# Performance work log

Hardware: AMD Instinct MI355X
Metric: run time of the kernel (lower is better)

## Reference

```python
import jax, jax.numpy as jnp
import numpy as np

N_NODES = 50000
N_EDGES = 1600000
HID = 128
REST = 96  # (hidden//4) x 1e vectors = 32*3
N_MP = 2


def _linear_init(key, fan_in, fan_out):
    return jax.random.normal(key, (fan_in, fan_out), dtype=jnp.float32) / np.sqrt(fan_in)


def setup_inputs() -> dict:
    key = jax.random.key(0)
    ks = jax.random.split(key, 16)
    h = jax.random.normal(ks[0], (N_NODES, HID + REST), dtype=jnp.float32)
    edge_index = jax.random.randint(ks[1], (2, N_EDGES), 0, N_NODES, dtype=jnp.int32)
    edge_len = jax.random.uniform(ks[2], (N_EDGES,), dtype=jnp.float32) * 5.0
    # ScalarMessagePassing MLPs: Linear(2*HID+1 -> HID), SiLU, Linear(HID -> HID), stacked per layer
    mp_w1 = jnp.stack([_linear_init(ks[3 + i], 2 * HID + 1, HID) for i in range(N_MP)])
    mp_b1 = jnp.zeros((N_MP, HID), dtype=jnp.float32)
    mp_w2 = jnp.stack([_linear_init(ks[5 + i], HID, HID) for i in range(N_MP)])
    mp_b2 = jnp.zeros((N_MP, HID), dtype=jnp.float32)
    # NodeUpdateMLP: Linear(HID -> HID), SiLU, Linear(HID -> HID)
    nu_w1 = _linear_init(ks[7], HID, HID)
    nu_b1 = jnp.zeros((HID,), dtype=jnp.float32)
    nu_w2 = _linear_init(ks[8], HID, HID)
    nu_b2 = jnp.zeros((HID,), dtype=jnp.float32)
    return dict(h=h, edge_index=edge_index, edge_len=edge_len,
                mp_w1=mp_w1, mp_b1=mp_b1, mp_w2=mp_w2, mp_b2=mp_b2,
                nu_w1=nu_w1, nu_b1=nu_b1, nu_w2=nu_w2, nu_b2=nu_b2)


def _scalar_mp(scalars, sender, receiver, edge_len, w1, b1, w2, b2):
    # gather -> MLP -> index_add scatter, residual on scalar channels
    msg_in = jnp.concatenate([scalars[sender], scalars[receiver], edge_len[:, None]], axis=-1)  # [E, 2H+1]
    msgs = jax.nn.silu(msg_in @ w1 + b1) @ w2 + b2  # [E, H]
    agg = jax.ops.segment_sum(msgs, receiver, num_segments=scalars.shape[0])  # [N, H]
    return scalars + agg


def reference(h, edge_index, edge_len, mp_w1, mp_b1, mp_w2, mp_b2, nu_w1, nu_b1, nu_w2, nu_b2):
    scalars, rest = h[..., :HID], h[..., HID:]
    sender, receiver = edge_index[0], edge_index[1]
    for i in range(N_MP):
        scalars = _scalar_mp(scalars, sender, receiver, edge_len,
                             mp_w1[i], mp_b1[i], mp_w2[i], mp_b2[i])
    # NodeUpdateMLP: scalars + MLP(scalars)
    scalars = scalars + (jax.nn.silu(scalars @ nu_w1 + nu_b1) @ nu_w2 + nu_b2)
    return jnp.concatenate([scalars, rest], axis=-1)
```

## Files before the change

### kernel.cpp

```cpp
#include <hip/hip_runtime.h>
#include <hip/hip_fp16.h>


#define NFEAT 224
#define RBITS 8
#define NB 196
#define CAP 10240
#define COPYB 512

typedef _Float16 v8h __attribute__((ext_vector_type(8)));
typedef _Float16 v2h __attribute__((ext_vector_type(2)));
typedef float f32x4 __attribute__((ext_vector_type(4)));

#define MFMA16(a, b, c) __builtin_amdgcn_mfma_f32_16x16x32_f16(a, b, c, 0, 0, 0)

__device__ __forceinline__ float silu_f(float x) {
    float e = __expf(-x);
    return x * __builtin_amdgcn_rcpf(1.0f + e);
}

__global__ void k_packbucket(const float* __restrict__ mp_w1, const float* __restrict__ mp_w2,
                             const float* __restrict__ nu_w1, const float* __restrict__ nu_w2,
                             _Float16* __restrict__ Wp,
                             const int* __restrict__ recv, const int* __restrict__ sender,
                             const float* __restrict__ elen, int* __restrict__ cnt,
                             uint2* __restrict__ bp, int E) {
    __shared__ int lhist[256];
    __shared__ int lcur[256];
    if (blockIdx.x < 8) {
        const float* srcs[8] = {
            mp_w1, mp_w1 + 16384, mp_w2,
            mp_w1 + 32896, mp_w1 + 32896 + 16384, mp_w2 + 16384,
            nu_w1, nu_w2
        };
        const float* W = srcs[blockIdx.x];
        _Float16* dst = Wp + (size_t)blockIdx.x * 16384;
        for (int i = 0; i < 8; ++i) {
            int u = threadIdx.x + i * 256;
            int nt = u >> 8;
            int kt = (u >> 6) & 3;
            int lane = u & 63;
            int kb = kt * 32 + (lane >> 4) * 8;
            int n = nt * 16 + (lane & 15);
#pragma unroll
            for (int j = 0; j < 8; ++j)
                dst[(size_t)u * 8 + j] = (_Float16)W[(size_t)(kb + j) * 128 + n];
        }
        return;
    }
    int t = threadIdx.x;
    int start = (blockIdx.x - 8) * 4096;
    int end = start + 4096; if (end > E) end = E;
    lhist[t] = 0;
    __syncthreads();
    int rv[16];
#pragma unroll
    for (int j = 0; j < 16; ++j) {
        int i = start + t + j * 256;
        rv[j] = (i < end) ? recv[i] : -1;
        if (rv[j] >= 0) atomicAdd(&lhist[rv[j] >> RBITS], 1);
    }
    __syncthreads();
    if (t < NB) {
        int c = lhist[t];
        lcur[t] = t * CAP + (c ? atomicAdd(&cnt[t], c) : 0);
    }
    __syncthreads();
#pragma unroll
    for (int j = 0; j < 16; ++j) {
        int i = start + t + j * 256;
        if (i < end) {
            int r = rv[j];
            int pos = atomicAdd(&lcur[r >> RBITS], 1);
            unsigned pay = (unsigned)sender[i] |
                           ((unsigned)__half_as_ushort(__float2half_rn(elen[i])) << 16);
            bp[pos] = make_uint2((unsigned)r, pay);
        }
    }
}


#define MM_STAGE_A_F32(Aptr, ldA)                                           \
    _Pragma("unroll") for (int i = 0; i < 4; ++i) {                         \
        int u = threadIdx.x + i * 256;                                      \
        int r = u >> 4;                                                     \
        int g = u & 15;                                                     \
        int gr = mm_bx * 64 + r;                                            \
        float4 x0 = make_float4(0.f, 0.f, 0.f, 0.f);                        \
        float4 x1 = x0;                                                     \
        if (gr < M) {                                                       \
            const float* s_ = (Aptr) + (size_t)gr * (ldA) + g * 8;          \
            x0 = *(const float4*)s_;                                        \
            x1 = *(const float4*)(s_ + 4);                                  \
        }                                                                   \
        v8h hv;                                                             \
        hv[0] = (_Float16)x0.x; hv[1] = (_Float16)x0.y;                     \
        hv[2] = (_Float16)x0.z; hv[3] = (_Float16)x0.w;                     \
        hv[4] = (_Float16)x1.x; hv[5] = (_Float16)x1.y;                     \
        hv[6] = (_Float16)x1.z; hv[7] = (_Float16)x1.w;                     \
        Af[((r >> 4) * 4 + (g >> 2)) * 64 + (g & 3) * 16 + (r & 15)] = hv;  \
    }

#define MM_STAGE_A_F16(Aptr)                                                \
    _Pragma("unroll") for (int i = 0; i < 4; ++i) {                         \
        int u = threadIdx.x + i * 256;                                      \
        int r = u >> 4;                                                     \
        int g = u & 15;                                                     \
        int gr = mm_bx * 64 + r;                                            \
        float4 x = make_float4(0.f, 0.f, 0.f, 0.f);                         \
        if (gr < M) x = *(const float4*)((Aptr) + (size_t)gr * 128 + g * 8);\
        *(float4*)&Af[((r >> 4) * 4 + (g >> 2)) * 64 + (g & 3) * 16 + (r & 15)] = x; \
    }

#define MM_WAVE_PROLOG                                                      \
    __syncthreads();                                                        \
    const int wv = threadIdx.x >> 6;                                        \
    const int lane = threadIdx.x & 63;                                      \
    const int q_ = lane >> 4;                                               \
    const int c0_ = lane & 15;                                              \
    v8h a0 = Af[(wv * 4 + 0) * 64 + lane];                                  \
    v8h a1 = Af[(wv * 4 + 1) * 64 + lane];                                  \
    v8h a2 = Af[(wv * 4 + 2) * 64 + lane];                                  \
    v8h a3 = Af[(wv * 4 + 3) * 64 + lane];                                  \
    const int grb = mm_bx * 64 + wv * 16 + q_ * 4;

#define MM_RELOAD_A(SRC)                                                    \
    a0 = SRC[(wv * 4 + 0) * 64 + lane];                                     \
    a1 = SRC[(wv * 4 + 1) * 64 + lane];                                     \
    a2 = SRC[(wv * 4 + 2) * 64 + lane];                                     \
    a3 = SRC[(wv * 4 + 3) * 64 + lane];

#define MM_COMPUTE_B(WPTR, ...)                                             \
    {                                                                       \
        const v8h* Bp_ = (const v8h*)(WPTR) + lane;                         \
        _Pragma("unroll") for (int nt = 0; nt < 8; ++nt) {                  \
            v8h b0 = Bp_[nt * 256];                                         \
            v8h b1v = Bp_[nt * 256 + 64];                                   \
            v8h b2v = Bp_[nt * 256 + 128];                                  \
            v8h b3v = Bp_[nt * 256 + 192];                                  \
            f32x4 c = {0.f, 0.f, 0.f, 0.f};                                 \
            c = MFMA16(a0, b0, c);                                          \
            c = MFMA16(a1, b1v, c);                                         \
            c = MFMA16(a2, b2v, c);                                         \
            c = MFMA16(a3, b3v, c);                                         \
            const int col = nt * 16 + c0_;                                  \
            __VA_ARGS__                                                     \
        }                                                                   \
    }

#define MM_EXCHANGE_IDX                                                     \
    int kt = col >> 5;                                                      \
    int o = col & 31;                                                       \
    int qp = o >> 3;                                                        \
    int j = o & 7;                                                          \
    int base = ((wv * 4 + kt) * 64 + qp * 16 + q_ * 4) * 8 + j;

__launch_bounds__(256)
__global__ void k_csr_xsrb_copy(const int* __restrict__ cnt, const uint2* __restrict__ bp,
                                int* __restrict__ deg, int* __restrict__ rowstart,
                                unsigned* __restrict__ epack,
                                const float* __restrict__ A,
                                const _Float16* __restrict__ Wp0, const float* __restrict__ b1,
                                _Float16* __restrict__ Xs, _Float16* __restrict__ Xrb, int M,
                                const float4* __restrict__ h4, float4* __restrict__ out4) {
    __shared__ v8h AfB[1024];
    const int gb = (M + 63) >> 6;
    if (blockIdx.x < NB) {
        int* hist = (int*)AfB;
        int* sh = hist + 256;
        int* lcur = sh + 256;
        int t = threadIdx.x;
        int b = blockIdx.x;
        int r0 = b << RBITS;
        int e0 = b * CAP;
        int e1 = e0 + cnt[b];
        hist[t] = 0;
        __syncthreads();
        for (int i = e0 + t; i < e1; i += 256)
            atomicAdd(&hist[(int)(bp[i].x & 255u)], 1);
        __syncthreads();
        sh[t] = hist[t];
        __syncthreads();
        for (int off = 1; off < 256; off <<= 1) {
            int add = (t >= off) ? sh[t - off] : 0;
            __syncthreads();
            sh[t] += add;
            __syncthreads();
        }
        int excl = (t == 0) ? 0 : sh[t - 1];
        lcur[t] = e0 + excl;
        int r = r0 + t;
        if (r < M) { deg[r] = hist[t]; rowstart[r] = e0 + excl; }
        __syncthreads();
        for (int i = e0 + t; i < e1; i += 256) {
            uint2 e = bp[i];
            int pos = atomicAdd(&lcur[(int)(e.x & 255u)], 1);
            epack[pos] = e.y;
        }
    } else if (blockIdx.x < NB + gb) {
        v8h* const Af = AfB;
        const int mm_bx = blockIdx.x - NB;
        MM_STAGE_A_F32(A, NFEAT)
        MM_WAVE_PROLOG
        MM_COMPUTE_B(Wp0, {
            _Pragma("unroll") for (int i = 0; i < 4; ++i) {
                int gr = grb + i;
                if (gr < M) Xs[(size_t)gr * 128 + col] = (_Float16)(c[i] * 0.5f);
            }
        })
        MM_COMPUTE_B(Wp0 + 16384, {
            float bc = b1[col];
            _Pragma("unroll") for (int i = 0; i < 4; ++i) {
                int gr = grb + i;
                if (gr < M) Xrb[(size_t)gr * 128 + col] = (_Float16)((c[i] + bc) * 0.5f);
            }
        })
    } else {
        int bid = blockIdx.x - NB - gb;
        int total = M * 24;
        for (int idx = bid * 256 + threadIdx.x; idx < total; idx += COPYB * 256) {
            int r = idx / 24;
            int c = idx - r * 24;
            out4[(size_t)r * 56 + 32 + c] = h4[(size_t)r * 56 + 32 + c];
        }
    }
}

__launch_bounds__(256)
__global__ void k_mm_accxsrb(const _Float16* __restrict__ P, const _Float16* __restrict__ Ww2,
                             const float* __restrict__ b2, const int* __restrict__ deg,
                             const float* __restrict__ Sin, int ldSin,
                             float* __restrict__ Sout,
                             const _Float16* __restrict__ Wp1, const float* __restrict__ b1,
                             _Float16* __restrict__ Xs, _Float16* __restrict__ Xrb, int M) {
    __shared__ v8h Af[1024];
    __shared__ v8h Af2[1024];
    const int mm_bx = blockIdx.x;
    MM_STAGE_A_F16(P)
    MM_WAVE_PROLOG
    _Float16* A2 = (_Float16*)Af2;
    MM_COMPUTE_B(Ww2, {
        float bc = b2[col];
        MM_EXCHANGE_IDX
        _Pragma("unroll") for (int i = 0; i < 4; ++i) {
            int gr = grb + i;
            float sv = 0.f;
            if (gr < M) {
                sv = Sin[(size_t)gr * ldSin + col] + c[i] + bc * (float)deg[gr];
                Sout[(size_t)gr * 128 + col] = sv;
            }
            A2[base + i * 8] = (_Float16)sv;
        }
    })
    __syncthreads();
    MM_RELOAD_A(Af2)
    MM_COMPUTE_B(Wp1, {
        _Pragma("unroll") for (int i = 0; i < 4; ++i) {
            int gr = grb + i;
            if (gr < M) Xs[(size_t)gr * 128 + col] = (_Float16)(c[i] * 0.5f);
        }
    })
    MM_COMPUTE_B(Wp1 + 16384, {
        float bc = b1[col];
        _Pragma("unroll") for (int i = 0; i < 4; ++i) {
            int gr = grb + i;
            if (gr < M) Xrb[(size_t)gr * 128 + col] = (_Float16)((c[i] + bc) * 0.5f);
        }
    })
}

__launch_bounds__(256)
__global__ void k_mm_accnode(const _Float16* __restrict__ P, const _Float16* __restrict__ Ww2,
                             const float* __restrict__ b2, const int* __restrict__ deg,
                             const float* __restrict__ Sin,
                             const _Float16* __restrict__ Wn1, const float* __restrict__ nb1,
                             const _Float16* __restrict__ Wn2, const float* __restrict__ nb2,
                             float* __restrict__ out, int M) {
    __shared__ v8h Af[1024];
    __shared__ v8h Af2[1024];
    const int mm_bx = blockIdx.x;
    MM_STAGE_A_F16(P)
    MM_WAVE_PROLOG
    float s2v[8][4];
    _Float16* A2 = (_Float16*)Af2;
    MM_COMPUTE_B(Ww2, {
        float bc = b2[col];
        MM_EXCHANGE_IDX
        _Pragma("unroll") for (int i = 0; i < 4; ++i) {
            int gr = grb + i;
            float sv = 0.f;
            if (gr < M) sv = Sin[(size_t)gr * 128 + col] + c[i] + bc * (float)deg[gr];
            s2v[nt][i] = sv;
            A2[base + i * 8] = (_Float16)sv;
        }
    })
    __syncthreads();
    MM_RELOAD_A(Af2)
    _Float16* A3 = (_Float16*)Af;
    MM_COMPUTE_B(Wn1, {
        float bc = nb1[col];
        MM_EXCHANGE_IDX
        _Pragma("unroll") for (int i = 0; i < 4; ++i)
            A3[base + i * 8] = (_Float16)silu_f(c[i] + bc);
    })
    __syncthreads();
    MM_RELOAD_A(Af)
    MM_COMPUTE_B(Wn2, {
        float bc = nb2[col];
        _Pragma("unroll") for (int i = 0; i < 4; ++i) {
            int gr = grb + i;
            if (gr < M)
                out[(size_t)gr * NFEAT + col] = s2v[nt][i] + c[i] + bc;
        }
    })
}

__device__ __forceinline__ v2h silu2_pk_h(v2h h) {
    const v2h hp3 = {(_Float16)3.f, (_Float16)3.f};
    const v2h hn3 = {(_Float16)-3.f, (_Float16)-3.f};
    v2h z = __builtin_elementwise_min(__builtin_elementwise_max(h, hn3), hp3);
    v2h w = z * z;
    v2h f = w * (_Float16)0.00033637f + (_Float16)-0.0074935f;
    f = f * w + (_Float16)0.063236f;
    f = f * w + (_Float16)-0.280292f;
    f = f * w + (_Float16)0.988137f;
    v2h u = z * f;
    return h * u + h;
}

__launch_bounds__(256)
__global__ void k_edge(const v2h* __restrict__ Xs, const v2h* __restrict__ Xrb,
                       const float* __restrict__ w1L, const unsigned* __restrict__ epack,
                       const int* __restrict__ rowstart, const int* __restrict__ deg,
                       v2h* __restrict__ P, int N) {
    int wid = (blockIdx.x * blockDim.x + threadIdx.x) >> 6;
    int lane = threadIdx.x & 63;
    if (wid >= N) return;
    int lo = __builtin_amdgcn_readfirstlane(rowstart[wid]);
    int dg = __builtin_amdgcn_readfirstlane(deg[wid]);
    const unsigned* ep = epack + lo;
    v2h xr = Xrb[(size_t)wid * 64 + lane];
    float2 wlf = *(const float2*)(w1L + lane * 2);
    v2h wl = {(_Float16)(wlf.x * 0.5f), (_Float16)(wlf.y * 0.5f)};
    float ax = 0.f, ay = 0.f;
    int k = 0;
    unsigned pc[8];
    v2h xc[8];
    if (dg >= 8) {
#pragma unroll
        for (int u = 0; u < 8; ++u) pc[u] = ep[u];
#pragma unroll
        for (int u = 0; u < 8; ++u)
            xc[u] = Xs[(size_t)(pc[u] & 0xFFFFu) * 64 + lane];
    }
    for (; k + 16 <= dg; k += 8) {
        unsigned pn[8];
        v2h xn[8];
#pragma unroll
        for (int u = 0; u < 8; ++u) pn[u] = ep[k + 8 + u];
#pragma unroll
        for (int u = 0; u < 8; ++u)
            xn[u] = Xs[(size_t)(pn[u] & 0xFFFFu) * 64 + lane];
        v2h t2 = {(_Float16)0.f, (_Float16)0.f};
#pragma unroll
        for (int u = 0; u < 8; ++u) {
            _Float16 lv = __builtin_bit_cast(_Float16, (unsigned short)(pc[u] >> 16));
            v2h h = xc[u] + xr + lv * wl;
            t2 = t2 + silu2_pk_h(h);
        }
        ax += (float)t2[0]; ay += (float)t2[1];
#pragma unroll
        for (int u = 0; u < 8; ++u) { pc[u] = pn[u]; xc[u] = xn[u]; }
    }
    if (k + 8 <= dg) {
        v2h t2 = {(_Float16)0.f, (_Float16)0.f};
#pragma unroll
        for (int u = 0; u < 8; ++u) {
            _Float16 lv = __builtin_bit_cast(_Float16, (unsigned short)(pc[u] >> 16));
            v2h h = xc[u] + xr + lv * wl;
            t2 = t2 + silu2_pk_h(h);
        }
        ax += (float)t2[0]; ay += (float)t2[1];
        k += 8;
    }
    for (; k < dg; ++k) {
        unsigned p = ep[k];
        _Float16 lv = __builtin_bit_cast(_Float16, (unsigned short)(p >> 16));
        v2h x = Xs[(size_t)(p & 0xFFFFu) * 64 + lane];
        v2h h = x + xr + lv * wl;
        v2h s = silu2_pk_h(h);
        ax += (float)s[0]; ay += (float)s[1];
    }
    v2h o = {(_Float16)ax, (_Float16)ay};
    P[(size_t)wid * 64 + lane] = o;
}

extern "C" void kernel_launch(void* const* d_in, const int* in_sizes, int n_in,
                              void* d_out, int out_size, void* d_ws, size_t ws_size,
                              hipStream_t stream) {
    const float* h      = (const float*)d_in[0];
    const int*   eidx   = (const int*)d_in[1];
    const float* elen   = (const float*)d_in[2];
    const float* mp_w1  = (const float*)d_in[3];
    const float* mp_b1  = (const float*)d_in[4];
    const float* mp_w2  = (const float*)d_in[5];
    const float* mp_b2  = (const float*)d_in[6];
    const float* nu_w1  = (const float*)d_in[7];
    const float* nu_b1  = (const float*)d_in[8];
    const float* nu_w2  = (const float*)d_in[9];
    const float* nu_b2  = (const float*)d_in[10];
    float* out = (float*)d_out;

    const int N = in_sizes[0] / NFEAT;
    const int E = in_sizes[2];
    const int* sender   = eidx;
    const int* receiver = eidx + E;

    char* w = (char*)d_ws;
    auto alloc = [&](size_t bytes) -> char* {
        char* p = w;
        w += (bytes + 255) & ~(size_t)255;
        return p;
    };
    float*    S1    = (float*)alloc((size_t)N * 128 * 4);
    _Float16* Pf    = (_Float16*)alloc((size_t)N * 128 * 2);
    _Float16* Xs16  = (_Float16*)alloc((size_t)N * 128 * 2);
    _Float16* Xrb16 = (_Float16*)alloc((size_t)N * 128 * 2);
    _Float16* Wp    = (_Float16*)alloc((size_t)8 * 16384 * 2);
    uint2*    bp    = (uint2*)alloc((size_t)NB * CAP * 8);
    unsigned* epack = (unsigned*)alloc((size_t)NB * CAP * 4);
    int*      deg      = (int*)alloc((size_t)N * 4);
    int*      rowstart = (int*)alloc((size_t)N * 4);
    int*      cnt      = (int*)alloc((size_t)NB * 4);

    (void)hipMemsetAsync(cnt, 0, (size_t)NB * 4, stream);

    const int gb = (N + 63) / 64;
    const int eb = (N * 64 + 255) / 256;
    const int bb = (E + 4095) / 4096;

    k_packbucket<<<8 + bb, 256, 0, stream>>>(mp_w1, mp_w2, nu_w1, nu_w2, Wp,
                                             receiver, sender, elen, cnt, bp, E);
    k_csr_xsrb_copy<<<NB + gb + COPYB, 256, 0, stream>>>(cnt, bp, deg, rowstart, epack,
                                                         h, Wp, mp_b1,
                                                         Xs16, Xrb16, N,
                                                         (const float4*)h, (float4*)out);
    k_edge<<<eb, 256, 0, stream>>>((const v2h*)Xs16, (const v2h*)Xrb16,
                                   mp_w1 + 32768, epack, rowstart, deg, (v2h*)Pf, N);
    k_mm_accxsrb<<<gb, 256, 0, stream>>>(Pf, Wp + (size_t)2 * 16384, mp_b2, deg,
                                         h, NFEAT, S1,
                                         Wp + (size_t)3 * 16384, mp_b1 + 128,
                                         Xs16, Xrb16, N);
    k_edge<<<eb, 256, 0, stream>>>((const v2h*)Xs16, (const v2h*)Xrb16,
                                   mp_w1 + 32896 + 32768, epack, rowstart, deg,
                                   (v2h*)Pf, N);
    k_mm_accnode<<<gb, 256, 0, stream>>>(Pf, Wp + (size_t)5 * 16384, mp_b2 + 128, deg,
                                         S1,
                                         Wp + (size_t)6 * 16384, nu_b1,
                                         Wp + (size_t)7 * 16384, nu_b2,
                                         out, N);
}
```

Before: 338.7 us.

## Store residual scalars in fp16 and use 512-thread blocks for node matmuls

```diff
diff --git a/kernel.cpp b/kernel.cpp
--- a/kernel.cpp
+++ b/kernel.cpp
@@ -80,7 +80,7 @@
 }
 
 
-#define MM_STAGE_A_F32(Aptr, ldA)                                           \
+#define MM_STAGE_A_F32_H16(Aptr, ldA, H16ptr)                               \
     _Pragma("unroll") for (int i = 0; i < 4; ++i) {                         \
         int u = threadIdx.x + i * 256;                                      \
         int r = u >> 4;                                                     \
@@ -98,18 +98,8 @@
         hv[2] = (_Float16)x0.z; hv[3] = (_Float16)x0.w;                     \
         hv[4] = (_Float16)x1.x; hv[5] = (_Float16)x1.y;                     \
         hv[6] = (_Float16)x1.z; hv[7] = (_Float16)x1.w;                     \
+        if (gr < M) *(v8h*)&(H16ptr)[(size_t)gr * 128 + g * 8] = hv;        \
         Af[((r >> 4) * 4 + (g >> 2)) * 64 + (g & 3) * 16 + (r & 15)] = hv;  \
-    }
-
-#define MM_STAGE_A_F16(Aptr)                                                \
-    _Pragma("unroll") for (int i = 0; i < 4; ++i) {                         \
-        int u = threadIdx.x + i * 256;                                      \
-        int r = u >> 4;                                                     \
-        int g = u & 15;                                                     \
-        int gr = mm_bx * 64 + r;                                            \
-        float4 x = make_float4(0.f, 0.f, 0.f, 0.f);                         \
-        if (gr < M) x = *(const float4*)((Aptr) + (size_t)gr * 128 + g * 8);\
-        *(float4*)&Af[((r >> 4) * 4 + (g >> 2)) * 64 + (g & 3) * 16 + (r & 15)] = x; \
     }
 
 #define MM_WAVE_PROLOG                                                      \
@@ -123,12 +113,6 @@
     v8h a2 = Af[(wv * 4 + 2) * 64 + lane];                                  \
     v8h a3 = Af[(wv * 4 + 3) * 64 + lane];                                  \
     const int grb = mm_bx * 64 + wv * 16 + q_ * 4;
-
-#define MM_RELOAD_A(SRC)                                                    \
-    a0 = SRC[(wv * 4 + 0) * 64 + lane];                                     \
-    a1 = SRC[(wv * 4 + 1) * 64 + lane];                                     \
-    a2 = SRC[(wv * 4 + 2) * 64 + lane];                                     \
-    a3 = SRC[(wv * 4 + 3) * 64 + lane];
 
 #define MM_COMPUTE_B(WPTR, ...)                                             \
     {                                                                       \
@@ -148,12 +132,63 @@
         }                                                                   \
     }
 
-#define MM_EXCHANGE_IDX                                                     \
+
+#define MM8_STAGE_A_F16(Aptr)                                               \
+    _Pragma("unroll") for (int i = 0; i < 2; ++i) {                         \
+        int u = threadIdx.x + i * 512;                                      \
+        int r = u >> 4;                                                     \
+        int g = u & 15;                                                     \
+        int gr = mm_bx * 64 + r;                                            \
+        float4 x = make_float4(0.f, 0.f, 0.f, 0.f);                         \
+        if (gr < M) x = *(const float4*)((Aptr) + (size_t)gr * 128 + g * 8);\
+        *(float4*)&Af[((r >> 4) * 4 + (g >> 2)) * 64 + (g & 3) * 16 + (r & 15)] = x; \
+    }
+
+#define MM8_WAVE_PROLOG                                                     \
+    __syncthreads();                                                        \
+    const int wv8 = threadIdx.x >> 6;                                       \
+    const int rq = wv8 & 3;                                                 \
+    const int nh = wv8 >> 2;                                                \
+    const int lane = threadIdx.x & 63;                                      \
+    const int q_ = lane >> 4;                                               \
+    const int c0_ = lane & 15;                                              \
+    v8h a0 = Af[(rq * 4 + 0) * 64 + lane];                                  \
+    v8h a1 = Af[(rq * 4 + 1) * 64 + lane];                                  \
+    v8h a2 = Af[(rq * 4 + 2) * 64 + lane];                                  \
+    v8h a3 = Af[(rq * 4 + 3) * 64 + lane];                                  \
+    const int grb = mm_bx * 64 + rq * 16 + q_ * 4;
+
+#define MM8_RELOAD_A(SRC)                                                   \
+    a0 = SRC[(rq * 4 + 0) * 64 + lane];                                     \
+    a1 = SRC[(rq * 4 + 1) * 64 + lane];                                     \
+    a2 = SRC[(rq * 4 + 2) * 64 + lane];                                     \
+    a3 = SRC[(rq * 4 + 3) * 64 + lane];
+
+#define MM8_COMPUTE_B(WPTR, ...)                                            \
+    {                                                                       \
+        const v8h* Bp_ = (const v8h*)(WPTR) + lane;                         \
+        _Pragma("unroll") for (int ntl = 0; ntl < 4; ++ntl) {               \
+            const int nt = nh * 4 + ntl;                                    \
+            v8h b0 = Bp_[nt * 256];                                         \
+            v8h b1v = Bp_[nt * 256 + 64];                                   \
+            v8h b2v = Bp_[nt * 256 + 128];                                  \
+            v8h b3v = Bp_[nt * 256 + 192];                                  \
+            f32x4 c = {0.f, 0.f, 0.f, 0.f};                                 \
+            c = MFMA16(a0, b0, c);                                          \
+            c = MFMA16(a1, b1v, c);                                         \
+            c = MFMA16(a2, b2v, c);                                         \
+            c = MFMA16(a3, b3v, c);                                         \
+            const int col = nt * 16 + c0_;                                  \
+            __VA_ARGS__                                                     \
+        }                                                                   \
+    }
+
+#define MM8_EXCHANGE_IDX                                                    \
     int kt = col >> 5;                                                      \
     int o = col & 31;                                                       \
     int qp = o >> 3;                                                        \
     int j = o & 7;                                                          \
-    int base = ((wv * 4 + kt) * 64 + qp * 16 + q_ * 4) * 8 + j;
+    int base = ((rq * 4 + kt) * 64 + qp * 16 + q_ * 4) * 8 + j;
 
 __launch_bounds__(256)
 __global__ void k_csr_xsrb_copy(const int* __restrict__ cnt, const uint2* __restrict__ bp,
@@ -161,7 +196,8 @@
                                 unsigned* __restrict__ epack,
                                 const float* __restrict__ A,
                                 const _Float16* __restrict__ Wp0, const float* __restrict__ b1,
-                                _Float16* __restrict__ Xs, _Float16* __restrict__ Xrb, int M,
+                                _Float16* __restrict__ Xs, _Float16* __restrict__ Xrb,
+                                _Float16* __restrict__ H16, int M,
                                 const float4* __restrict__ h4, float4* __restrict__ out4) {
     __shared__ v8h AfB[1024];
     const int gb = (M + 63) >> 6;
@@ -200,7 +236,7 @@
     } else if (blockIdx.x < NB + gb) {
         v8h* const Af = AfB;
         const int mm_bx = blockIdx.x - NB;
-        MM_STAGE_A_F32(A, NFEAT)
+        MM_STAGE_A_F32_H16(A, NFEAT, H16)
         MM_WAVE_PROLOG
         MM_COMPUTE_B(Wp0, {
             _Pragma("unroll") for (int i = 0; i < 4; ++i) {
@@ -226,41 +262,41 @@
     }
 }
 
-__launch_bounds__(256)
+__launch_bounds__(512)
 __global__ void k_mm_accxsrb(const _Float16* __restrict__ P, const _Float16* __restrict__ Ww2,
                              const float* __restrict__ b2, const int* __restrict__ deg,
-                             const float* __restrict__ Sin, int ldSin,
-                             float* __restrict__ Sout,
+                             const _Float16* __restrict__ Sin16,
+                             _Float16* __restrict__ S1h,
                              const _Float16* __restrict__ Wp1, const float* __restrict__ b1,
                              _Float16* __restrict__ Xs, _Float16* __restrict__ Xrb, int M) {
     __shared__ v8h Af[1024];
     __shared__ v8h Af2[1024];
     const int mm_bx = blockIdx.x;
-    MM_STAGE_A_F16(P)
-    MM_WAVE_PROLOG
+    MM8_STAGE_A_F16(P)
+    MM8_WAVE_PROLOG
     _Float16* A2 = (_Float16*)Af2;
-    MM_COMPUTE_B(Ww2, {
+    MM8_COMPUTE_B(Ww2, {
         float bc = b2[col];
-        MM_EXCHANGE_IDX
+        MM8_EXCHANGE_IDX
         _Pragma("unroll") for (int i = 0; i < 4; ++i) {
             int gr = grb + i;
             float sv = 0.f;
             if (gr < M) {
-                sv = Sin[(size_t)gr * ldSin + col] + c[i] + bc * (float)deg[gr];
-                Sout[(size_t)gr * 128 + col] = sv;
+                sv = (float)Sin16[(size_t)gr * 128 + col] + c[i] + bc * (float)deg[gr];
+                S1h[(size_t)gr * 128 + col] = (_Float16)sv;
             }
             A2[base + i * 8] = (_Float16)sv;
         }
     })
     __syncthreads();
-    MM_RELOAD_A(Af2)
-    MM_COMPUTE_B(Wp1, {
+    MM8_RELOAD_A(Af2)
+    MM8_COMPUTE_B(Wp1, {
         _Pragma("unroll") for (int i = 0; i < 4; ++i) {
             int gr = grb + i;
             if (gr < M) Xs[(size_t)gr * 128 + col] = (_Float16)(c[i] * 0.5f);
         }
     })
-    MM_COMPUTE_B(Wp1 + 16384, {
+    MM8_COMPUTE_B(Wp1 + 16384, {
         float bc = b1[col];
         _Pragma("unroll") for (int i = 0; i < 4; ++i) {
             int gr = grb + i;
@@ -269,48 +305,48 @@
     })
 }
 
-__launch_bounds__(256)
+__launch_bounds__(512)
 __global__ void k_mm_accnode(const _Float16* __restrict__ P, const _Float16* __restrict__ Ww2,
                              const float* __restrict__ b2, const int* __restrict__ deg,
-                             const float* __restrict__ Sin,
+                             const _Float16* __restrict__ Sin16,
                              const _Float16* __restrict__ Wn1, const float* __restrict__ nb1,
                              const _Float16* __restrict__ Wn2, const float* __restrict__ nb2,
                              float* __restrict__ out, int M) {
     __shared__ v8h Af[1024];
     __shared__ v8h Af2[1024];
     const int mm_bx = blockIdx.x;
-    MM_STAGE_A_F16(P)
-    MM_WAVE_PROLOG
-    float s2v[8][4];
+    MM8_STAGE_A_F16(P)
+    MM8_WAVE_PROLOG
+    float s2v[4][4];
     _Float16* A2 = (_Float16*)Af2;
-    MM_COMPUTE_B(Ww2, {
+    MM8_COMPUTE_B(Ww2, {
         float bc = b2[col];
-        MM_EXCHANGE_IDX
+        MM8_EXCHANGE_IDX
         _Pragma("unroll") for (int i = 0; i < 4; ++i) {
             int gr = grb + i;
             float sv = 0.f;
-            if (gr < M) sv = Sin[(size_t)gr * 128 + col] + c[i] + bc * (float)deg[gr];
-            s2v[nt][i] = sv;
+            if (gr < M) sv = (float)Sin16[(size_t)gr * 128 + col] + c[i] + bc * (float)deg[gr];
+            s2v[ntl][i] = sv;
             A2[base + i * 8] = (_Float16)sv;
         }
     })
     __syncthreads();
-    MM_RELOAD_A(Af2)
+    MM8_RELOAD_A(Af2)
     _Float16* A3 = (_Float16*)Af;
-    MM_COMPUTE_B(Wn1, {
+    MM8_COMPUTE_B(Wn1, {
         float bc = nb1[col];
-        MM_EXCHANGE_IDX
+        MM8_EXCHANGE_IDX
         _Pragma("unroll") for (int i = 0; i < 4; ++i)
             A3[base + i * 8] = (_Float16)silu_f(c[i] + bc);
     })
     __syncthreads();
-    MM_RELOAD_A(Af)
-    MM_COMPUTE_B(Wn2, {
+    MM8_RELOAD_A(Af)
+    MM8_COMPUTE_B(Wn2, {
         float bc = nb2[col];
         _Pragma("unroll") for (int i = 0; i < 4; ++i) {
             int gr = grb + i;
             if (gr < M)
-                out[(size_t)gr * NFEAT + col] = s2v[nt][i] + c[i] + bc;
+                out[(size_t)gr * NFEAT + col] = s2v[ntl][i] + c[i] + bc;
         }
     })
 }
@@ -422,7 +458,8 @@
         w += (bytes + 255) & ~(size_t)255;
         return p;
     };
-    float*    S1    = (float*)alloc((size_t)N * 128 * 4);
+    _Float16* S1h   = (_Float16*)alloc((size_t)N * 128 * 2);
+    _Float16* H16   = (_Float16*)alloc((size_t)N * 128 * 2);
     _Float16* Pf    = (_Float16*)alloc((size_t)N * 128 * 2);
     _Float16* Xs16  = (_Float16*)alloc((size_t)N * 128 * 2);
     _Float16* Xrb16 = (_Float16*)alloc((size_t)N * 128 * 2);
@@ -443,19 +480,19 @@
                                              receiver, sender, elen, cnt, bp, E);
     k_csr_xsrb_copy<<<NB + gb + COPYB, 256, 0, stream>>>(cnt, bp, deg, rowstart, epack,
                                                          h, Wp, mp_b1,
-                                                         Xs16, Xrb16, N,
+                                                         Xs16, Xrb16, H16, N,
                                                          (const float4*)h, (float4*)out);
     k_edge<<<eb, 256, 0, stream>>>((const v2h*)Xs16, (const v2h*)Xrb16,
                                    mp_w1 + 32768, epack, rowstart, deg, (v2h*)Pf, N);
-    k_mm_accxsrb<<<gb, 256, 0, stream>>>(Pf, Wp + (size_t)2 * 16384, mp_b2, deg,
-                                         h, NFEAT, S1,
+    k_mm_accxsrb<<<gb, 512, 0, stream>>>(Pf, Wp + (size_t)2 * 16384, mp_b2, deg,
+                                         H16, S1h,
                                          Wp + (size_t)3 * 16384, mp_b1 + 128,
                                          Xs16, Xrb16, N);
     k_edge<<<eb, 256, 0, stream>>>((const v2h*)Xs16, (const v2h*)Xrb16,
                                    mp_w1 + 32896 + 32768, epack, rowstart, deg,
                                    (v2h*)Pf, N);
-    k_mm_accnode<<<gb, 256, 0, stream>>>(Pf, Wp + (size_t)5 * 16384, mp_b2 + 128, deg,
-                                         S1,
+    k_mm_accnode<<<gb, 512, 0, stream>>>(Pf, Wp + (size_t)5 * 16384, mp_b2 + 128, deg,
+                                         S1h,
                                          Wp + (size_t)6 * 16384, nu_b1,
                                          Wp + (size_t)7 * 16384, nu_b2,
                                          out, N);
```

Measured after the change: 338.2 us. Within noise of the previous version (-0.2%).

## Fuse edge and node-MLP stages into one cooperative persistent kernel with grid syncs

Applied to the files above, without the earlier changes.

```diff
diff --git a/kernel.cpp b/kernel.cpp
--- a/kernel.cpp
+++ b/kernel.cpp
@@ -1,5 +1,8 @@
 #include <hip/hip_runtime.h>
 #include <hip/hip_fp16.h>
+#include <hip/hip_cooperative_groups.h>
+
+namespace cg = cooperative_groups;
 
 
 #define NFEAT 224
@@ -80,7 +83,7 @@
 }
 
 
-#define MM_STAGE_A_F32(Aptr, ldA)                                           \
+#define MM_STAGE_A_F32_H16(Aptr, ldA, H16ptr)                               \
     _Pragma("unroll") for (int i = 0; i < 4; ++i) {                         \
         int u = threadIdx.x + i * 256;                                      \
         int r = u >> 4;                                                     \
@@ -98,6 +101,7 @@
         hv[2] = (_Float16)x0.z; hv[3] = (_Float16)x0.w;                     \
         hv[4] = (_Float16)x1.x; hv[5] = (_Float16)x1.y;                     \
         hv[6] = (_Float16)x1.z; hv[7] = (_Float16)x1.w;                     \
+        if (gr < M) *(v8h*)&(H16ptr)[(size_t)gr * 128 + g * 8] = hv;        \
         Af[((r >> 4) * 4 + (g >> 2)) * 64 + (g & 3) * 16 + (r & 15)] = hv;  \
     }
 
@@ -161,7 +165,8 @@
                                 unsigned* __restrict__ epack,
                                 const float* __restrict__ A,
                                 const _Float16* __restrict__ Wp0, const float* __restrict__ b1,
-                                _Float16* __restrict__ Xs, _Float16* __restrict__ Xrb, int M,
+                                _Float16* __restrict__ Xs, _Float16* __restrict__ Xrb,
+                                _Float16* __restrict__ H16, int M,
                                 const float4* __restrict__ h4, float4* __restrict__ out4) {
     __shared__ v8h AfB[1024];
     const int gb = (M + 63) >> 6;
@@ -200,7 +205,7 @@
     } else if (blockIdx.x < NB + gb) {
         v8h* const Af = AfB;
         const int mm_bx = blockIdx.x - NB;
-        MM_STAGE_A_F32(A, NFEAT)
+        MM_STAGE_A_F32_H16(A, NFEAT, H16)
         MM_WAVE_PROLOG
         MM_COMPUTE_B(Wp0, {
             _Pragma("unroll") for (int i = 0; i < 4; ++i) {
@@ -226,95 +231,6 @@
     }
 }
 
-__launch_bounds__(256)
-__global__ void k_mm_accxsrb(const _Float16* __restrict__ P, const _Float16* __restrict__ Ww2,
-                             const float* __restrict__ b2, const int* __restrict__ deg,
-                             const float* __restrict__ Sin, int ldSin,
-                             float* __restrict__ Sout,
-                             const _Float16* __restrict__ Wp1, const float* __restrict__ b1,
-                             _Float16* __restrict__ Xs, _Float16* __restrict__ Xrb, int M) {
-    __shared__ v8h Af[1024];
-    __shared__ v8h Af2[1024];
-    const int mm_bx = blockIdx.x;
-    MM_STAGE_A_F16(P)
-    MM_WAVE_PROLOG
-    _Float16* A2 = (_Float16*)Af2;
-    MM_COMPUTE_B(Ww2, {
-        float bc = b2[col];
-        MM_EXCHANGE_IDX
-        _Pragma("unroll") for (int i = 0; i < 4; ++i) {
-            int gr = grb + i;
-            float sv = 0.f;
-            if (gr < M) {
-                sv = Sin[(size_t)gr * ldSin + col] + c[i] + bc * (float)deg[gr];
-                Sout[(size_t)gr * 128 + col] = sv;
-            }
-            A2[base + i * 8] = (_Float16)sv;
-        }
-    })
-    __syncthreads();
-    MM_RELOAD_A(Af2)
-    MM_COMPUTE_B(Wp1, {
-        _Pragma("unroll") for (int i = 0; i < 4; ++i) {
-            int gr = grb + i;
-            if (gr < M) Xs[(size_t)gr * 128 + col] = (_Float16)(c[i] * 0.5f);
-        }
-    })
-    MM_COMPUTE_B(Wp1 + 16384, {
-        float bc = b1[col];
-        _Pragma("unroll") for (int i = 0; i < 4; ++i) {
-            int gr = grb + i;
-            if (gr < M) Xrb[(size_t)gr * 128 + col] = (_Float16)((c[i] + bc) * 0.5f);
-        }
-    })
-}
-
-__launch_bounds__(256)
-__global__ void k_mm_accnode(const _Float16* __restrict__ P, const _Float16* __restrict__ Ww2,
-                             const float* __restrict__ b2, const int* __restrict__ deg,
-                             const float* __restrict__ Sin,
-                             const _Float16* __restrict__ Wn1, const float* __restrict__ nb1,
-                             const _Float16* __restrict__ Wn2, const float* __restrict__ nb2,
-                             float* __restrict__ out, int M) {
-    __shared__ v8h Af[1024];
-    __shared__ v8h Af2[1024];
-    const int mm_bx = blockIdx.x;
-    MM_STAGE_A_F16(P)
-    MM_WAVE_PROLOG
-    float s2v[8][4];
-    _Float16* A2 = (_Float16*)Af2;
-    MM_COMPUTE_B(Ww2, {
-        float bc = b2[col];
-        MM_EXCHANGE_IDX
-        _Pragma("unroll") for (int i = 0; i < 4; ++i) {
-            int gr = grb + i;
-            float sv = 0.f;
-            if (gr < M) sv = Sin[(size_t)gr * 128 + col] + c[i] + bc * (float)deg[gr];
-            s2v[nt][i] = sv;
-            A2[base + i * 8] = (_Float16)sv;
-        }
-    })
-    __syncthreads();
-    MM_RELOAD_A(Af2)
-    _Float16* A3 = (_Float16*)Af;
-    MM_COMPUTE_B(Wn1, {
-        float bc = nb1[col];
-        MM_EXCHANGE_IDX
-        _Pragma("unroll") for (int i = 0; i < 4; ++i)
-            A3[base + i * 8] = (_Float16)silu_f(c[i] + bc);
-    })
-    __syncthreads();
-    MM_RELOAD_A(Af)
-    MM_COMPUTE_B(Wn2, {
-        float bc = nb2[col];
-        _Pragma("unroll") for (int i = 0; i < 4; ++i) {
-            int gr = grb + i;
-            if (gr < M)
-                out[(size_t)gr * NFEAT + col] = s2v[nt][i] + c[i] + bc;
-        }
-    })
-}
-
 __device__ __forceinline__ v2h silu2_pk_h(v2h h) {
     const v2h hp3 = {(_Float16)3.f, (_Float16)3.f};
     const v2h hn3 = {(_Float16)-3.f, (_Float16)-3.f};
@@ -328,20 +244,14 @@
     return h * u + h;
 }
 
-__launch_bounds__(256)
-__global__ void k_edge(const v2h* __restrict__ Xs, const v2h* __restrict__ Xrb,
-                       const float* __restrict__ w1L, const unsigned* __restrict__ epack,
-                       const int* __restrict__ rowstart, const int* __restrict__ deg,
-                       v2h* __restrict__ P, int N) {
-    int wid = (blockIdx.x * blockDim.x + threadIdx.x) >> 6;
-    int lane = threadIdx.x & 63;
-    if (wid >= N) return;
+__device__ __forceinline__ void edge_one_row(int wid, int lane,
+        const v2h* __restrict__ Xs, const v2h* __restrict__ Xrb, v2h wl,
+        const unsigned* __restrict__ epack, const int* __restrict__ rowstart,
+        const int* __restrict__ deg, v2h* __restrict__ P) {
     int lo = __builtin_amdgcn_readfirstlane(rowstart[wid]);
     int dg = __builtin_amdgcn_readfirstlane(deg[wid]);
     const unsigned* ep = epack + lo;
     v2h xr = Xrb[(size_t)wid * 64 + lane];
-    float2 wlf = *(const float2*)(w1L + lane * 2);
-    v2h wl = {(_Float16)(wlf.x * 0.5f), (_Float16)(wlf.y * 0.5f)};
     float ax = 0.f, ay = 0.f;
     int k = 0;
     unsigned pc[8];
@@ -393,6 +303,138 @@
     }
     v2h o = {(_Float16)ax, (_Float16)ay};
     P[(size_t)wid * 64 + lane] = o;
+}
+
+__device__ __forceinline__ void accxsrb_block(
+    const int mm_bx, v8h* const Af,
+    const _Float16* __restrict__ P, const _Float16* __restrict__ Ww2,
+    const float* __restrict__ b2, const int* __restrict__ deg,
+    const _Float16* __restrict__ Sin16, _Float16* __restrict__ S1h,
+    const _Float16* __restrict__ Wp1, const float* __restrict__ b1,
+    _Float16* __restrict__ Xs, _Float16* __restrict__ Xrb, const int M) {
+    __syncthreads();
+    MM_STAGE_A_F16(P)
+    MM_WAVE_PROLOG
+    __syncthreads();
+    _Float16* A2 = (_Float16*)Af;
+    MM_COMPUTE_B(Ww2, {
+        float bc = b2[col];
+        MM_EXCHANGE_IDX
+        _Pragma("unroll") for (int i = 0; i < 4; ++i) {
+            int gr = grb + i;
+            float sv = 0.f;
+            if (gr < M) {
+                sv = (float)Sin16[(size_t)gr * 128 + col] + c[i] + bc * (float)deg[gr];
+                S1h[(size_t)gr * 128 + col] = (_Float16)sv;
+            }
+            A2[base + i * 8] = (_Float16)sv;
+        }
+    })
+    __syncthreads();
+    MM_RELOAD_A(Af)
+    MM_COMPUTE_B(Wp1, {
+        _Pragma("unroll") for (int i = 0; i < 4; ++i) {
+            int gr = grb + i;
+            if (gr < M) Xs[(size_t)gr * 128 + col] = (_Float16)(c[i] * 0.5f);
+        }
+    })
+    MM_COMPUTE_B(Wp1 + 16384, {
+        float bc = b1[col];
+        _Pragma("unroll") for (int i = 0; i < 4; ++i) {
+            int gr = grb + i;
+            if (gr < M) Xrb[(size_t)gr * 128 + col] = (_Float16)((c[i] + bc) * 0.5f);
+        }
+    })
+}
+
+__device__ __forceinline__ void accnode_block(
+    const int mm_bx, v8h* const Af,
+    const _Float16* __restrict__ P, const _Float16* __restrict__ Ww2,
+    const float* __restrict__ b2, const int* __restrict__ deg,
+    _Float16* __restrict__ S1h,
+    const _Float16* __restrict__ Wn1, const float* __restrict__ nb1,
+    const _Float16* __restrict__ Wn2, const float* __restrict__ nb2,
+    float* __restrict__ out, const int M) {
+    __syncthreads();
+    MM_STAGE_A_F16(P)
+    MM_WAVE_PROLOG
+    __syncthreads();
+    _Float16* A2 = (_Float16*)Af;
+    MM_COMPUTE_B(Ww2, {
+        float bc = b2[col];
+        MM_EXCHANGE_IDX
+        _Pragma("unroll") for (int i = 0; i < 4; ++i) {
+            int gr = grb + i;
+            float sv = 0.f;
+            if (gr < M) {
+                sv = (float)S1h[(size_t)gr * 128 + col] + c[i] + bc * (float)deg[gr];
+                S1h[(size_t)gr * 128 + col] = (_Float16)sv;
+            }
+            A2[base + i * 8] = (_Float16)sv;
+        }
+    })
+    __syncthreads();
+    MM_RELOAD_A(Af)
+    __syncthreads();
+    MM_COMPUTE_B(Wn1, {
+        float bc = nb1[col];
+        MM_EXCHANGE_IDX
+        _Pragma("unroll") for (int i = 0; i < 4; ++i)
+            A2[base + i * 8] = (_Float16)silu_f(c[i] + bc);
+    })
+    __syncthreads();
+    MM_RELOAD_A(Af)
+    MM_COMPUTE_B(Wn2, {
+        float bc = nb2[col];
+        _Pragma("unroll") for (int i = 0; i < 4; ++i) {
+            int gr = grb + i;
+            if (gr < M)
+                out[(size_t)gr * NFEAT + col] =
+                    (float)S1h[(size_t)gr * 128 + col] + c[i] + bc;
+        }
+    })
+}
+
+__launch_bounds__(256, 6)
+__global__ void k_tail(_Float16* Xs, _Float16* Xrb,
+                       const float* w1L0, const float* w1L1,
+                       const unsigned* epack, const int* rowstart, const int* deg,
+                       _Float16* Pf,
+                       const _Float16* Ww2_0, const float* b2_0,
+                       const _Float16* Wp1, const float* b1_1,
+                       const _Float16* H16, _Float16* S1h,
+                       const _Float16* Ww2_1, const float* b2_1,
+                       const _Float16* Wn1, const float* nb1,
+                       const _Float16* Wn2, const float* nb2,
+                       float* out, int N) {
+    cg::grid_group grid = cg::this_grid();
+    __shared__ v8h Af[1024];
+    const int lane = threadIdx.x & 63;
+    const int gw = gridDim.x * 4;
+    const int w0 = blockIdx.x * 4 + (threadIdx.x >> 6);
+    const int gb = (N + 63) >> 6;
+
+    {
+        float2 wlf = *(const float2*)(w1L0 + lane * 2);
+        v2h wl = {(_Float16)(wlf.x * 0.5f), (_Float16)(wlf.y * 0.5f)};
+        for (int wid = w0; wid < N; wid += gw)
+            edge_one_row(wid, lane, (const v2h*)Xs, (const v2h*)Xrb, wl,
+                         epack, rowstart, deg, (v2h*)Pf);
+    }
+    grid.sync();
+    for (int bx = blockIdx.x; bx < gb; bx += gridDim.x)
+        accxsrb_block(bx, Af, Pf, Ww2_0, b2_0, deg, H16, S1h, Wp1, b1_1, Xs, Xrb, N);
+    grid.sync();
+    {
+        float2 wlf = *(const float2*)(w1L1 + lane * 2);
+        v2h wl = {(_Float16)(wlf.x * 0.5f), (_Float16)(wlf.y * 0.5f)};
+        for (int wid = w0; wid < N; wid += gw)
+            edge_one_row(wid, lane, (const v2h*)Xs, (const v2h*)Xrb, wl,
+                         epack, rowstart, deg, (v2h*)Pf);
+    }
+    grid.sync();
+    for (int bx = blockIdx.x; bx < gb; bx += gridDim.x)
+        accnode_block(bx, Af, Pf, Ww2_1, b2_1, deg, S1h, Wn1, nb1, Wn2, nb2, out, N);
 }
 
 extern "C" void kernel_launch(void* const* d_in, const int* in_sizes, int n_in,
@@ -422,7 +464,8 @@
         w += (bytes + 255) & ~(size_t)255;
         return p;
     };
-    float*    S1    = (float*)alloc((size_t)N * 128 * 4);
+    _Float16* S1h   = (_Float16*)alloc((size_t)N * 128 * 2);
+    _Float16* H16   = (_Float16*)alloc((size_t)N * 128 * 2);
     _Float16* Pf    = (_Float16*)alloc((size_t)N * 128 * 2);
     _Float16* Xs16  = (_Float16*)alloc((size_t)N * 128 * 2);
     _Float16* Xrb16 = (_Float16*)alloc((size_t)N * 128 * 2);
@@ -436,27 +479,49 @@
     (void)hipMemsetAsync(cnt, 0, (size_t)NB * 4, stream);
 
     const int gb = (N + 63) / 64;
-    const int eb = (N * 64 + 255) / 256;
     const int bb = (E + 4095) / 4096;
 
     k_packbucket<<<8 + bb, 256, 0, stream>>>(mp_w1, mp_w2, nu_w1, nu_w2, Wp,
                                              receiver, sender, elen, cnt, bp, E);
     k_csr_xsrb_copy<<<NB + gb + COPYB, 256, 0, stream>>>(cnt, bp, deg, rowstart, epack,
                                                          h, Wp, mp_b1,
-                                                         Xs16, Xrb16, N,
+                                                         Xs16, Xrb16, H16, N,
                                                          (const float4*)h, (float4*)out);
-    k_edge<<<eb, 256, 0, stream>>>((const v2h*)Xs16, (const v2h*)Xrb16,
-                                   mp_w1 + 32768, epack, rowstart, deg, (v2h*)Pf, N);
-    k_mm_accxsrb<<<gb, 256, 0, stream>>>(Pf, Wp + (size_t)2 * 16384, mp_b2, deg,
-                                         h, NFEAT, S1,
-                                         Wp + (size_t)3 * 16384, mp_b1 + 128,
-                                         Xs16, Xrb16, N);
-    k_edge<<<eb, 256, 0, stream>>>((const v2h*)Xs16, (const v2h*)Xrb16,
-                                   mp_w1 + 32896 + 32768, epack, rowstart, deg,
-                                   (v2h*)Pf, N);
-    k_mm_accnode<<<gb, 256, 0, stream>>>(Pf, Wp + (size_t)5 * 16384, mp_b2 + 128, deg,
-                                         S1,
-                                         Wp + (size_t)6 * 16384, nu_b1,
-                                         Wp + (size_t)7 * 16384, nu_b2,
-                                         out, N);
-}
+
+    _Float16* a_Xs = Xs16;
+    _Float16* a_Xrb = Xrb16;
+    const float* a_w1L0 = mp_w1 + 32768;
+    const float* a_w1L1 = mp_w1 + 32896 + 32768;
+    const unsigned* a_ep = epack;
+    const int* a_rs = rowstart;
+    const int* a_dg = deg;
+    _Float16* a_Pf = Pf;
+    const _Float16* a_Ww20 = Wp + (size_t)2 * 16384;
+    const float* a_b20 = mp_b2;
+    const _Float16* a_Wp1 = Wp + (size_t)3 * 16384;
+    const float* a_b11 = mp_b1 + 128;
+    const _Float16* a_H16 = H16;
+    _Float16* a_S1h = S1h;
+    const _Float16* a_Ww21 = Wp + (size_t)5 * 16384;
+    const float* a_b21 = mp_b2 + 128;
+    const _Float16* a_Wn1 = Wp + (size_t)6 * 16384;
+    const float* a_nb1 = nu_b1;
+    const _Float16* a_Wn2 = Wp + (size_t)7 * 16384;
+    const float* a_nb2 = nu_b2;
+    float* a_out = out;
+    int a_N = N;
+    void* targs[22] = {
+        &a_Xs, &a_Xrb, (void*)&a_w1L0, (void*)&a_w1L1,
+        (void*)&a_ep, (void*)&a_rs, (void*)&a_dg, &a_Pf,
+        (void*)&a_Ww20, (void*)&a_b20, (void*)&a_Wp1, (void*)&a_b11,
+        (void*)&a_H16, &a_S1h, (void*)&a_Ww21, (void*)&a_b21,
+        (void*)&a_Wn1, (void*)&a_nb1, (void*)&a_Wn2, (void*)&a_nb2,
+        &a_out, &a_N
+    };
+    int maxb = 0;
+    if (hipOccupancyMaxActiveBlocksPerMultiprocessor(&maxb, k_tail, 256, 0) != hipSuccess
+        || maxb < 1) maxb = 4;
+    if (maxb > 8) maxb = 8;
+    int tgrid = maxb * 256;
+    (void)hipLaunchCooperativeKernel(k_tail, dim3(tgrid), dim3(256), targs, 0, stream);
+}
```

After: 910.2 us. 169% more time.
